# Performance work log

Measured on AMD Instinct MI355X. Metric: run time of the kernel, lower is better.

The kernel has to match this reference:

```python
import jax, jax.numpy as jnp
import numpy as np

B, S, D, H, DK, DV = 2, 2048, 1024, 16, 64, 64
NEG_INF = -2.0**32 + 1.0  # matches torch module's self.inf


def setup_inputs() -> dict:
    key = jax.random.key(0)
    ks = jax.random.split(key, 9)
    sc = 0.02
    x = jax.random.normal(ks[0], (B, S, D), jnp.float32)
    Wq = jax.random.normal(ks[1], (D, H * DK), jnp.float32) * sc
    bq = jax.random.normal(ks[2], (H * DK,), jnp.float32) * sc
    Wk = jax.random.normal(ks[3], (D, H * DK), jnp.float32) * sc
    bk = jax.random.normal(ks[4], (H * DK,), jnp.float32) * sc
    Wv = jax.random.normal(ks[5], (D, H * DV), jnp.float32) * sc
    bv = jax.random.normal(ks[6], (H * DV,), jnp.float32) * sc
    Wo = jax.random.normal(ks[7], (H * DV, D), jnp.float32) * sc
    bo = jax.random.normal(ks[8], (D,), jnp.float32) * sc
    return {"x": x, "Wq": Wq, "bq": bq, "Wk": Wk, "bk": bk,
            "Wv": Wv, "bv": bv, "Wo": Wo, "bo": bo}


def reference(x, Wq, bq, Wk, bk, Wv, bv, Wo, bo):
    # stage == 'train' path: causal mask applied.
    b, s, _ = x.shape
    # chunk(heads, dim=-1) + cat(dim=0) in torch == per-head split; equivalent
    # math expressed as [B, S, H, d] with head-batched einsums.
    q = (x @ Wq + bq).reshape(b, s, H, DK)
    k = (x @ Wk + bk).reshape(b, s, H, DK)
    v = (x @ Wv + bv).reshape(b, s, H, DV)
    # NOTE: original module does NOT scale by 1/sqrt(dk) — stay faithful.
    score = jnp.einsum('bqhd,bkhd->bhqk', q, k)  # [B, H, S, S]
    causal = jnp.tril(jnp.ones((s, s), dtype=bool))
    score = jnp.where(causal, score, NEG_INF)
    attn = jax.nn.softmax(score, axis=-1)
    ctx = jnp.einsum('bhqk,bkhd->bqhd', attn, v).reshape(b, s, H * DV)
    return ctx @ Wo + bo
```

## Files before the change

kernel.cpp:

```cpp
#include <hip/hip_runtime.h>
#include <stdint.h>

typedef unsigned short u16;
typedef __bf16 bf16_t;
typedef bf16_t bf16x8 __attribute__((ext_vector_type(8)));
typedef float f32x4 __attribute__((ext_vector_type(4)));

#define SB 2048
#define DMODEL 1024
#define NH 16
#define HD 64

__device__ __forceinline__ u16 f2bf(float f) {
  union { float f; uint32_t u; } v; v.f = f;
  uint32_t u = v.u;
  return (u16)((u + 0x7FFFu + ((u >> 16) & 1u)) >> 16);
}

__device__ __forceinline__ void gload16(const void* g, void* l) {
  __builtin_amdgcn_global_load_lds((const __attribute__((address_space(1))) void*)g,
                                   (__attribute__((address_space(3))) void*)l, 16, 0, 0);
}


__global__ __launch_bounds__(256) void k_cvt_x(const float* __restrict__ x, u16* __restrict__ xb) {
  int i = blockIdx.x * 256 + threadIdx.x;
  float4 v = ((const float4*)x)[i];
  uint2 o;
  o.x = (unsigned)f2bf(v.x) | ((unsigned)f2bf(v.y) << 16);
  o.y = (unsigned)f2bf(v.z) | ((unsigned)f2bf(v.w) << 16);
  ((uint2*)xb)[i] = o;
}

__global__ __launch_bounds__(256) void k_transpose_w(
    const float* __restrict__ W0, const float* __restrict__ W1,
    const float* __restrict__ W2, const float* __restrict__ W3,
    u16* __restrict__ T0, u16* __restrict__ T1,
    u16* __restrict__ T2, u16* __restrict__ T3) {
  __shared__ float tile[32][33];
  int mat = blockIdx.z;
  const float* W = (mat == 0) ? W0 : (mat == 1) ? W1 : (mat == 2) ? W2 : W3;
  u16* T = (mat == 0) ? T0 : (mat == 1) ? T1 : (mat == 2) ? T2 : T3;
  int r0 = blockIdx.y * 32, c0 = blockIdx.x * 32;
  int tx = threadIdx.x & 31, ty = threadIdx.x >> 5;
#pragma unroll
  for (int j = 0; j < 4; ++j)
    tile[ty + j * 8][tx] = W[(size_t)(r0 + ty + j * 8) * DMODEL + c0 + tx];
  __syncthreads();
#pragma unroll
  for (int j = 0; j < 4; ++j)
    T[(size_t)(c0 + ty + j * 8) * DMODEL + r0 + tx] = f2bf(tile[tx][ty + j * 8]);
}


__device__ __forceinline__ void gemm_loop(const u16* __restrict__ A, const u16* __restrict__ Bt,
                                          u16* As, u16* Bs, f32x4 (&acc)[4][4], int m0) {
  const int t = threadIdx.x, w = t >> 6, lane = t & 63;
  const int l15 = lane & 15, grp = lane >> 4;
  const int wr = w >> 1, wc = w & 1;
#pragma unroll
  for (int i = 0; i < 4; ++i)
#pragma unroll
    for (int j = 0; j < 4; ++j) acc[i][j] = (f32x4){0.f, 0.f, 0.f, 0.f};

  for (int ks = 0; ks < 16; ++ks) {
    const int k0 = ks * 64;
#pragma unroll
    for (int j = 0; j < 4; ++j) {
      int glin = (w * 4 + j) * 64 + lane;
      int row = glin >> 3;
      int g = (glin & 7) ^ (row & 7);
      gload16(A + (size_t)(m0 + row) * DMODEL + k0 + g * 8, (char*)As + (size_t)(w * 4 + j) * 1024);
      gload16(Bt + (size_t)row * DMODEL + k0 + g * 8, (char*)Bs + (size_t)(w * 4 + j) * 1024);
    }
    __syncthreads();
#pragma unroll
    for (int kk = 0; kk < 2; ++kk) {
      bf16x8 af[4], bfr[4];
#pragma unroll
      for (int i = 0; i < 4; ++i) {
        int row = wr * 64 + i * 16 + l15;
        int g = (4 * kk + grp) ^ (row & 7);
        af[i] = *(const bf16x8*)((const char*)As + row * 128 + (g << 4));
      }
#pragma unroll
      for (int j = 0; j < 4; ++j) {
        int row = wc * 64 + j * 16 + l15;
        int g = (4 * kk + grp) ^ (row & 7);
        bfr[j] = *(const bf16x8*)((const char*)Bs + row * 128 + (g << 4));
      }
#pragma unroll
      for (int i = 0; i < 4; ++i)
#pragma unroll
        for (int j = 0; j < 4; ++j)
          acc[i][j] = __builtin_amdgcn_mfma_f32_16x16x32_bf16(af[i], bfr[j], acc[i][j], 0, 0, 0);
    }
    __syncthreads();
  }
}

__global__ __launch_bounds__(256) void k_gemm_qk(
    const u16* __restrict__ xb,
    const u16* __restrict__ WqT, const u16* __restrict__ WkT,
    const float* __restrict__ bq, const float* __restrict__ bk,
    u16* __restrict__ Qg, u16* __restrict__ Kg) {
  __shared__ u16 As[128 * 64];
  __shared__ u16 Bs[128 * 64];
  const int nt = blockIdx.x, mt = blockIdx.y;
  const int mat = nt >> 3, n0 = (nt & 7) * 128;
  const u16* Bt = mat ? WkT : WqT;
  const float* bias = mat ? bk : bq;
  u16* out = mat ? Kg : Qg;

  f32x4 acc[4][4];
  gemm_loop(xb, Bt + (size_t)n0 * DMODEL, As, Bs, acc, mt * 128);

  const int t = threadIdx.x, w = t >> 6, lane = t & 63;
  const int l15 = lane & 15, grp = lane >> 4;
  const int wr = w >> 1, wc = w & 1;
#pragma unroll
  for (int i = 0; i < 4; ++i)
#pragma unroll
    for (int j = 0; j < 4; ++j)
#pragma unroll
      for (int r = 0; r < 4; ++r) {
        int mrow = mt * 128 + wr * 64 + i * 16 + 4 * grp + r;
        int ncol = n0 + wc * 64 + j * 16 + l15;
        float v = acc[i][j][r] + bias[ncol];
        int b = mrow >> 11, s2 = mrow & 2047, h = ncol >> 6, d2 = ncol & 63;
        out[((((size_t)b * NH + h) * SB + s2) << 6) + d2] = f2bf(v);
      }
}

__global__ __launch_bounds__(256) void k_gemm_vt(
    const u16* __restrict__ xb, const u16* __restrict__ WvT,
    const float* __restrict__ bv, u16* __restrict__ VTg) {
  __shared__ u16 As[128 * 64];
  __shared__ u16 Bs[128 * 64];
  const int nt = blockIdx.x, mt = blockIdx.y;
  const int n0 = nt * 128;

  f32x4 acc[4][4];
  gemm_loop(WvT, xb + (size_t)n0 * DMODEL, As, Bs, acc, mt * 128);

  const int t = threadIdx.x, w = t >> 6, lane = t & 63;
  const int l15 = lane & 15, grp = lane >> 4;
  const int wr = w >> 1, wc = w & 1;
#pragma unroll
  for (int i = 0; i < 4; ++i)
#pragma unroll
    for (int j = 0; j < 4; ++j)
#pragma unroll
      for (int r = 0; r < 4; ++r) {
        int mrow = mt * 128 + wr * 64 + i * 16 + 4 * grp + r;
        int ncol = n0 + wc * 64 + j * 16 + l15;
        float v = acc[i][j][r] + bv[mrow];
        int b2 = ncol >> 11, key = ncol & 2047, h2 = mrow >> 6, vc = mrow & 63;
        VTg[((((size_t)b2 * NH + h2) << 6) + vc) * 2048 + key] = f2bf(v);
      }
}

__global__ __launch_bounds__(256) void k_gemm_o(
    const u16* __restrict__ ctx, const u16* __restrict__ WoT,
    const float* __restrict__ bo, float* __restrict__ out) {
  __shared__ u16 As[128 * 64];
  __shared__ u16 Bs[128 * 64];
  const int nt = blockIdx.x, mt = blockIdx.y;
  const int n0 = nt * 128;

  f32x4 acc[4][4];
  gemm_loop(ctx, WoT + (size_t)n0 * DMODEL, As, Bs, acc, mt * 128);

  const int t = threadIdx.x, w = t >> 6, lane = t & 63;
  const int l15 = lane & 15, grp = lane >> 4;
  const int wr = w >> 1, wc = w & 1;
#pragma unroll
  for (int i = 0; i < 4; ++i)
#pragma unroll
    for (int j = 0; j < 4; ++j)
#pragma unroll
      for (int r = 0; r < 4; ++r) {
        int mrow = mt * 128 + wr * 64 + i * 16 + 4 * grp + r;
        int ncol = n0 + wc * 64 + j * 16 + l15;
        out[(size_t)mrow * DMODEL + ncol] = acc[i][j][r] + bo[ncol];
      }
}


__global__ __launch_bounds__(256) void k_flash(const u16* __restrict__ Qg,
                                               const u16* __restrict__ Kg,
                                               const u16* __restrict__ VTg,
                                               u16* __restrict__ ctx) {
  __shared__ u16 Ks[2][64 * 64];
  __shared__ u16 VTs[2][64 * 64];
  __shared__ u16 Ps[4][16 * 64];
  const int pi = blockIdx.x, bh = blockIdx.y;
  const int t = threadIdx.x, w = t >> 6, lane = t & 63;
  const int l15 = lane & 15, grp = lane >> 4;
  const size_t bhS = (size_t)bh * SB;
  const u16* Kb = Kg + (bhS << 6);
  const u16* Vb = VTg + (bhS << 6);
  const int b = bh >> 4, h = bh & 15;

#pragma unroll 1
  for (int ph = 0; ph < 2; ++ph) {
    const int qt = ph ? 31 - pi : pi;
    const int qb = qt * 64;
    bf16x8 qf[2];
#pragma unroll
    for (int c = 0; c < 2; ++c)
      qf[c] = *(const bf16x8*)(Qg + ((bhS + qb + w * 16 + l15) << 6) + 32 * c + 8 * grp);
    f32x4 acc[4];
    float plsum[4];
#pragma unroll
    for (int ct = 0; ct < 4; ++ct) acc[ct] = (f32x4){0.f, 0.f, 0.f, 0.f};
#pragma unroll
    for (int j = 0; j < 4; ++j) plsum[j] = 0.f;

#pragma unroll
    for (int j = 0; j < 2; ++j) {
      int glin = w * 128 + j * 64 + lane;
      int row = glin >> 3;
      int g = (glin & 7) ^ (row & 7);
      gload16(Kb + ((size_t)row << 6) + g * 8, (char*)Ks[0] + w * 2048 + j * 1024);
      gload16(Vb + ((size_t)row << 11) + g * 8, (char*)VTs[0] + w * 2048 + j * 1024);
    }
    __syncthreads();
    int cur = 0;
    for (int kt = 0; kt <= qt; ++kt) {
      if (kt < qt) {
        const int kb2 = (kt + 1) * 64;
#pragma unroll
        for (int j = 0; j < 2; ++j) {
          int glin = w * 128 + j * 64 + lane;
          int row = glin >> 3;
          int g = (glin & 7) ^ (row & 7);
          gload16(Kb + ((size_t)(kb2 + row) << 6) + g * 8,
                  (char*)Ks[cur ^ 1] + w * 2048 + j * 1024);
          gload16(Vb + ((size_t)row << 11) + kb2 + g * 8,
                  (char*)VTs[cur ^ 1] + w * 2048 + j * 1024);
        }
      }
      f32x4 sc[4];
#pragma unroll
      for (int ct = 0; ct < 4; ++ct) {
        sc[ct] = (f32x4){0.f, 0.f, 0.f, 0.f};
#pragma unroll
        for (int c = 0; c < 2; ++c) {
          int row = ct * 16 + l15;
          int g = (4 * c + grp) ^ (row & 7);
          bf16x8 kf = *(const bf16x8*)((const char*)Ks[cur] + row * 128 + (g << 4));
          sc[ct] = __builtin_amdgcn_mfma_f32_16x16x32_bf16(qf[c], kf, sc[ct], 0, 0, 0);
        }
      }
      if (kt == qt) {
#pragma unroll
        for (int ct = 0; ct < 4; ++ct)
#pragma unroll
          for (int j = 0; j < 4; ++j) {
            int key = ct * 16 + l15, r = w * 16 + 4 * grp + j;
            if (key > r) sc[ct][j] = -1e30f;
          }
      }
#pragma unroll
      for (int ct = 0; ct < 4; ++ct)
#pragma unroll
        for (int j = 0; j < 4; ++j) {
          float p = __expf(sc[ct][j] - 32.0f);
          plsum[j] += p;
          int r = 4 * grp + j, cc = ct * 16 + l15;
          *(u16*)((char*)Ps[w] + r * 128 + (((cc >> 3) ^ (r & 7)) << 4) + (cc & 7) * 2) = f2bf(p);
        }
      asm volatile("s_waitcnt lgkmcnt(0)" ::: "memory");
      __builtin_amdgcn_sched_barrier(0);
#pragma unroll
      for (int ct = 0; ct < 4; ++ct) {
#pragma unroll
        for (int c2 = 0; c2 < 2; ++c2) {
          int pg = (4 * c2 + grp) ^ (l15 & 7);
          bf16x8 pf = *(const bf16x8*)((const char*)Ps[w] + l15 * 128 + (pg << 4));
          int vrow = ct * 16 + l15;
          int vg = (4 * c2 + grp) ^ (vrow & 7);
          bf16x8 vf = *(const bf16x8*)((const char*)VTs[cur] + vrow * 128 + (vg << 4));
          acc[ct] = __builtin_amdgcn_mfma_f32_16x16x32_bf16(pf, vf, acc[ct], 0, 0, 0);
        }
      }
      __syncthreads();
      cur ^= 1;
    }
#pragma unroll
    for (int j = 0; j < 4; ++j) {
#pragma unroll
      for (int d = 1; d < 16; d <<= 1) plsum[j] += __shfl_xor(plsum[j], d, 64);
      float inv = 1.f / plsum[j];
      int rg = qb + w * 16 + 4 * grp + j;
#pragma unroll
      for (int ct = 0; ct < 4; ++ct) {
        int col = h * 64 + ct * 16 + l15;
        ctx[((size_t)b * SB + rg) * DMODEL + col] = f2bf(acc[ct][j] * inv);
      }
    }
  }
}


extern "C" void kernel_launch(void* const* d_in, const int* in_sizes, int n_in,
                              void* d_out, int out_size, void* d_ws, size_t ws_size,
                              hipStream_t stream) {
  const float* x  = (const float*)d_in[0];
  const float* Wq = (const float*)d_in[1];
  const float* bq = (const float*)d_in[2];
  const float* Wk = (const float*)d_in[3];
  const float* bk = (const float*)d_in[4];
  const float* Wv = (const float*)d_in[5];
  const float* bv = (const float*)d_in[6];
  const float* Wo = (const float*)d_in[7];
  const float* bo = (const float*)d_in[8];
  float* out = (float*)d_out;

  char* ws = (char*)d_ws;
  u16* xb  = (u16*)(ws);
  u16* WqT = (u16*)(ws + (8ull  << 20));
  u16* WkT = (u16*)(ws + (10ull << 20));
  u16* WvT = (u16*)(ws + (12ull << 20));
  u16* WoT = (u16*)(ws + (14ull << 20));
  u16* Qg  = (u16*)(ws + (16ull << 20));
  u16* Kg  = (u16*)(ws + (24ull << 20));
  u16* VTg = (u16*)(ws + (32ull << 20));
  u16* ctx = (u16*)(ws + (40ull << 20));

  hipLaunchKernelGGL(k_cvt_x, dim3(4096), dim3(256), 0, stream, x, xb);
  hipLaunchKernelGGL(k_transpose_w, dim3(32, 32, 4), dim3(256), 0, stream,
                     Wq, Wk, Wv, Wo, WqT, WkT, WvT, WoT);
  hipLaunchKernelGGL(k_gemm_qk, dim3(16, 32), dim3(256), 0, stream,
                     xb, WqT, WkT, bq, bk, Qg, Kg);
  hipLaunchKernelGGL(k_gemm_vt, dim3(32, 8), dim3(256), 0, stream, xb, WvT, bv, VTg);
  hipLaunchKernelGGL(k_flash, dim3(16, 32), dim3(256), 0, stream, Qg, Kg, VTg, ctx);
  hipLaunchKernelGGL(k_gemm_o, dim3(8, 32), dim3(256), 0, stream, ctx, WoT, bo, out);
}
```

Baseline: 128.3 us.

## Double-buffer GEMM loads, merge QKV GEMMs, and widen flash blocks

The GEMM main loop now double-buffers its LDS tiles, so the next K-slice's global-to-LDS loads are issued before the MFMAs on the current slice. This replaces the old load-sync-compute pattern. The Q/K and V^T projection GEMMs are merged into one 768-block launch with a swizzled block id meant to group blocks per XCD. The flash attention kernel now uses 512 threads covering a 128-row query tile, with per-wave causal masking and an XCD-aware mapping from block to (batch, head). Together these aim to hide load latency, cut launch overhead and improve L2 locality, at the cost of doubled LDS per block and a larger flash block that may lower occupancy.

```diff
diff --git a/kernel.cpp b/kernel.cpp
--- a/kernel.cpp
+++ b/kernel.cpp
@@ -53,8 +53,8 @@
 }
 
 
-__device__ __forceinline__ void gemm_loop(const u16* __restrict__ A, const u16* __restrict__ Bt,
-                                          u16* As, u16* Bs, f32x4 (&acc)[4][4], int m0) {
+__device__ __forceinline__ void gemm_db(const u16* __restrict__ A, const u16* __restrict__ Bt,
+                                        u16* As, u16* Bs, f32x4 (&acc)[4][4]) {
   const int t = threadIdx.x, w = t >> 6, lane = t & 63;
   const int l15 = lane & 15, grp = lane >> 4;
   const int wr = w >> 1, wc = w & 1;
@@ -63,17 +63,25 @@
 #pragma unroll
     for (int j = 0; j < 4; ++j) acc[i][j] = (f32x4){0.f, 0.f, 0.f, 0.f};
 
+#define STAGE_G(BUF, K0)                                                                     \
+  do {                                                                                       \
+    _Pragma("unroll") for (int j_ = 0; j_ < 4; ++j_) {                                       \
+      int glin_ = (w * 4 + j_) * 64 + lane;                                                  \
+      int row_ = glin_ >> 3;                                                                 \
+      int g_ = (glin_ & 7) ^ (row_ & 7);                                                     \
+      gload16(A + (size_t)row_ * DMODEL + (K0) + g_ * 8,                                     \
+              (char*)As + (BUF) * 16384 + glin_ * 16);                                       \
+      gload16(Bt + (size_t)row_ * DMODEL + (K0) + g_ * 8,                                    \
+              (char*)Bs + (BUF) * 16384 + glin_ * 16);                                       \
+    }                                                                                        \
+  } while (0)
+
+  STAGE_G(0, 0);
+  __syncthreads();
+  int cur = 0;
+#pragma unroll 1
   for (int ks = 0; ks < 16; ++ks) {
-    const int k0 = ks * 64;
-#pragma unroll
-    for (int j = 0; j < 4; ++j) {
-      int glin = (w * 4 + j) * 64 + lane;
-      int row = glin >> 3;
-      int g = (glin & 7) ^ (row & 7);
-      gload16(A + (size_t)(m0 + row) * DMODEL + k0 + g * 8, (char*)As + (size_t)(w * 4 + j) * 1024);
-      gload16(Bt + (size_t)row * DMODEL + k0 + g * 8, (char*)Bs + (size_t)(w * 4 + j) * 1024);
-    }
-    __syncthreads();
+    if (ks < 15) STAGE_G(cur ^ 1, (ks + 1) * 64);
 #pragma unroll
     for (int kk = 0; kk < 2; ++kk) {
       bf16x8 af[4], bfr[4];
@@ -81,13 +89,13 @@
       for (int i = 0; i < 4; ++i) {
         int row = wr * 64 + i * 16 + l15;
         int g = (4 * kk + grp) ^ (row & 7);
-        af[i] = *(const bf16x8*)((const char*)As + row * 128 + (g << 4));
+        af[i] = *(const bf16x8*)((const char*)As + cur * 16384 + row * 128 + (g << 4));
       }
 #pragma unroll
       for (int j = 0; j < 4; ++j) {
         int row = wc * 64 + j * 16 + l15;
         int g = (4 * kk + grp) ^ (row & 7);
-        bfr[j] = *(const bf16x8*)((const char*)Bs + row * 128 + (g << 4));
+        bfr[j] = *(const bf16x8*)((const char*)Bs + cur * 16384 + row * 128 + (g << 4));
       }
 #pragma unroll
       for (int i = 0; i < 4; ++i)
@@ -96,24 +104,40 @@
           acc[i][j] = __builtin_amdgcn_mfma_f32_16x16x32_bf16(af[i], bfr[j], acc[i][j], 0, 0, 0);
     }
     __syncthreads();
+    cur ^= 1;
   }
-}
-
-__global__ __launch_bounds__(256) void k_gemm_qk(
-    const u16* __restrict__ xb,
-    const u16* __restrict__ WqT, const u16* __restrict__ WkT,
-    const float* __restrict__ bq, const float* __restrict__ bk,
-    u16* __restrict__ Qg, u16* __restrict__ Kg) {
-  __shared__ u16 As[128 * 64];
-  __shared__ u16 Bs[128 * 64];
-  const int nt = blockIdx.x, mt = blockIdx.y;
-  const int mat = nt >> 3, n0 = (nt & 7) * 128;
-  const u16* Bt = mat ? WkT : WqT;
-  const float* bias = mat ? bk : bq;
-  u16* out = mat ? Kg : Qg;
+#undef STAGE_G
+}
+
+
+__global__ __launch_bounds__(256) void k_qkv(
+    const u16* __restrict__ xb, const u16* __restrict__ WqT, const u16* __restrict__ WkT,
+    const u16* __restrict__ WvT, const float* __restrict__ bq, const float* __restrict__ bk,
+    const float* __restrict__ bv, u16* __restrict__ Qg, u16* __restrict__ Kg,
+    u16* __restrict__ VTg) {
+  __shared__ u16 As[2][8192];
+  __shared__ u16 Bs[2][8192];
+  int id = blockIdx.x;
+  id = (id & 7) * 96 + (id >> 3);
+  const int role = id >> 8;
+  int mt, nt;
+  const u16 *Abase, *Bbase;
+  if (role < 2) {
+    int r = id & 255;
+    mt = r >> 3;
+    nt = r & 7;
+    Abase = xb + (size_t)mt * 128 * DMODEL;
+    Bbase = (role ? WkT : WqT) + (size_t)nt * 128 * DMODEL;
+  } else {
+    int r = id & 255;
+    mt = r >> 5;
+    nt = r & 31;
+    Abase = WvT + (size_t)mt * 128 * DMODEL;
+    Bbase = xb + (size_t)nt * 128 * DMODEL;
+  }
 
   f32x4 acc[4][4];
-  gemm_loop(xb, Bt + (size_t)n0 * DMODEL, As, Bs, acc, mt * 128);
+  gemm_db(Abase, Bbase, As[0], Bs[0], acc);
 
   const int t = threadIdx.x, w = t >> 6, lane = t & 63;
   const int l15 = lane & 15, grp = lane >> 4;
@@ -124,24 +148,32 @@
     for (int j = 0; j < 4; ++j)
 #pragma unroll
       for (int r = 0; r < 4; ++r) {
-        int mrow = mt * 128 + wr * 64 + i * 16 + 4 * grp + r;
-        int ncol = n0 + wc * 64 + j * 16 + l15;
-        float v = acc[i][j][r] + bias[ncol];
-        int b = mrow >> 11, s2 = mrow & 2047, h = ncol >> 6, d2 = ncol & 63;
-        out[((((size_t)b * NH + h) * SB + s2) << 6) + d2] = f2bf(v);
-      }
-}
-
-__global__ __launch_bounds__(256) void k_gemm_vt(
-    const u16* __restrict__ xb, const u16* __restrict__ WvT,
-    const float* __restrict__ bv, u16* __restrict__ VTg) {
-  __shared__ u16 As[128 * 64];
-  __shared__ u16 Bs[128 * 64];
+        int mr = mt * 128 + wr * 64 + i * 16 + 4 * grp + r;
+        int nc = nt * 128 + wc * 64 + j * 16 + l15;
+        float v = acc[i][j][r];
+        if (role < 2) {
+          float vb = v + (role ? bk[nc] : bq[nc]);
+          int b_ = mr >> 11, s_ = mr & 2047, h_ = nc >> 6, d_ = nc & 63;
+          u16* out = role ? Kg : Qg;
+          out[((((size_t)b_ * NH + h_) * SB + s_) << 6) + d_] = f2bf(vb);
+        } else {
+          float vb = v + bv[mr];
+          int b2 = nc >> 11, key = nc & 2047, h2 = mr >> 6, vc = mr & 63;
+          VTg[((((size_t)b2 * NH + h2) << 6) + vc) * SB + key] = f2bf(vb);
+        }
+      }
+}
+
+
+__global__ __launch_bounds__(256) void k_gemm_o(
+    const u16* __restrict__ ctx, const u16* __restrict__ WoT,
+    const float* __restrict__ bo, float* __restrict__ out) {
+  __shared__ u16 As[2][8192];
+  __shared__ u16 Bs[2][8192];
   const int nt = blockIdx.x, mt = blockIdx.y;
-  const int n0 = nt * 128;
 
   f32x4 acc[4][4];
-  gemm_loop(WvT, xb + (size_t)n0 * DMODEL, As, Bs, acc, mt * 128);
+  gemm_db(ctx + (size_t)mt * 128 * DMODEL, WoT + (size_t)nt * 128 * DMODEL, As[0], Bs[0], acc);
 
   const int t = threadIdx.x, w = t >> 6, lane = t & 63;
   const int l15 = lane & 15, grp = lane >> 4;
@@ -153,48 +185,23 @@
 #pragma unroll
       for (int r = 0; r < 4; ++r) {
         int mrow = mt * 128 + wr * 64 + i * 16 + 4 * grp + r;
-        int ncol = n0 + wc * 64 + j * 16 + l15;
-        float v = acc[i][j][r] + bv[mrow];
-        int b2 = ncol >> 11, key = ncol & 2047, h2 = mrow >> 6, vc = mrow & 63;
-        VTg[((((size_t)b2 * NH + h2) << 6) + vc) * 2048 + key] = f2bf(v);
-      }
-}
-
-__global__ __launch_bounds__(256) void k_gemm_o(
-    const u16* __restrict__ ctx, const u16* __restrict__ WoT,
-    const float* __restrict__ bo, float* __restrict__ out) {
-  __shared__ u16 As[128 * 64];
-  __shared__ u16 Bs[128 * 64];
-  const int nt = blockIdx.x, mt = blockIdx.y;
-  const int n0 = nt * 128;
-
-  f32x4 acc[4][4];
-  gemm_loop(ctx, WoT + (size_t)n0 * DMODEL, As, Bs, acc, mt * 128);
-
-  const int t = threadIdx.x, w = t >> 6, lane = t & 63;
-  const int l15 = lane & 15, grp = lane >> 4;
-  const int wr = w >> 1, wc = w & 1;
-#pragma unroll
-  for (int i = 0; i < 4; ++i)
-#pragma unroll
-    for (int j = 0; j < 4; ++j)
-#pragma unroll
-      for (int r = 0; r < 4; ++r) {
-        int mrow = mt * 128 + wr * 64 + i * 16 + 4 * grp + r;
-        int ncol = n0 + wc * 64 + j * 16 + l15;
+        int ncol = nt * 128 + wc * 64 + j * 16 + l15;
         out[(size_t)mrow * DMODEL + ncol] = acc[i][j][r] + bo[ncol];
       }
 }
 
 
-__global__ __launch_bounds__(256) void k_flash(const u16* __restrict__ Qg,
+__global__ __launch_bounds__(512) void k_flash(const u16* __restrict__ Qg,
                                                const u16* __restrict__ Kg,
                                                const u16* __restrict__ VTg,
                                                u16* __restrict__ ctx) {
-  __shared__ u16 Ks[2][64 * 64];
-  __shared__ u16 VTs[2][64 * 64];
-  __shared__ u16 Ps[4][16 * 64];
-  const int pi = blockIdx.x, bh = blockIdx.y;
+  __shared__ u16 Ks[2][4096];
+  __shared__ u16 VTs[2][4096];
+  __shared__ u16 Ps[8][1024];
+  const int linb = blockIdx.x;
+  const int xcd = linb & 7, idx = linb >> 3;
+  const int bh = xcd + ((idx & 3) << 3);
+  const int pi = idx >> 2;
   const int t = threadIdx.x, w = t >> 6, lane = t & 63;
   const int l15 = lane & 15, grp = lane >> 4;
   const size_t bhS = (size_t)bh * SB;
@@ -204,8 +211,9 @@
 
 #pragma unroll 1
   for (int ph = 0; ph < 2; ++ph) {
-    const int qt = ph ? 31 - pi : pi;
-    const int qb = qt * 64;
+    const int qt = ph ? 15 - pi : pi;
+    const int qb = qt * 128;
+    const int nkt = 2 * qt + 2;
     bf16x8 qf[2];
 #pragma unroll
     for (int c = 0; c < 2; ++c)
@@ -217,29 +225,20 @@
 #pragma unroll
     for (int j = 0; j < 4; ++j) plsum[j] = 0.f;
 
-#pragma unroll
-    for (int j = 0; j < 2; ++j) {
-      int glin = w * 128 + j * 64 + lane;
-      int row = glin >> 3;
-      int g = (glin & 7) ^ (row & 7);
-      gload16(Kb + ((size_t)row << 6) + g * 8, (char*)Ks[0] + w * 2048 + j * 1024);
-      gload16(Vb + ((size_t)row << 11) + g * 8, (char*)VTs[0] + w * 2048 + j * 1024);
+    {
+      int row = t >> 3, g = (t & 7) ^ (row & 7);
+      gload16(Kb + ((size_t)row << 6) + g * 8, (char*)Ks[0] + t * 16);
+      gload16(Vb + ((size_t)row << 11) + g * 8, (char*)VTs[0] + t * 16);
     }
     __syncthreads();
     int cur = 0;
-    for (int kt = 0; kt <= qt; ++kt) {
-      if (kt < qt) {
-        const int kb2 = (kt + 1) * 64;
-#pragma unroll
-        for (int j = 0; j < 2; ++j) {
-          int glin = w * 128 + j * 64 + lane;
-          int row = glin >> 3;
-          int g = (glin & 7) ^ (row & 7);
-          gload16(Kb + ((size_t)(kb2 + row) << 6) + g * 8,
-                  (char*)Ks[cur ^ 1] + w * 2048 + j * 1024);
-          gload16(Vb + ((size_t)row << 11) + kb2 + g * 8,
-                  (char*)VTs[cur ^ 1] + w * 2048 + j * 1024);
-        }
+    for (int kt = 0; kt < nkt; ++kt) {
+      const int kb = kt * 64;
+      if (kt + 1 < nkt) {
+        int row = t >> 3, g = (t & 7) ^ (row & 7);
+        int kb2 = kb + 64;
+        gload16(Kb + ((size_t)(kb2 + row) << 6) + g * 8, (char*)Ks[cur ^ 1] + t * 16);
+        gload16(Vb + ((size_t)row << 11) + kb2 + g * 8, (char*)VTs[cur ^ 1] + t * 16);
       }
       f32x4 sc[4];
 #pragma unroll
@@ -253,12 +252,12 @@
           sc[ct] = __builtin_amdgcn_mfma_f32_16x16x32_bf16(qf[c], kf, sc[ct], 0, 0, 0);
         }
       }
-      if (kt == qt) {
+      if (kb + 63 >= qb + w * 16) {
 #pragma unroll
         for (int ct = 0; ct < 4; ++ct)
 #pragma unroll
           for (int j = 0; j < 4; ++j) {
-            int key = ct * 16 + l15, r = w * 16 + 4 * grp + j;
+            int key = kb + ct * 16 + l15, r = qb + w * 16 + 4 * grp + j;
             if (key > r) sc[ct][j] = -1e30f;
           }
       }
@@ -332,9 +331,8 @@
   hipLaunchKernelGGL(k_cvt_x, dim3(4096), dim3(256), 0, stream, x, xb);
   hipLaunchKernelGGL(k_transpose_w, dim3(32, 32, 4), dim3(256), 0, stream,
                      Wq, Wk, Wv, Wo, WqT, WkT, WvT, WoT);
-  hipLaunchKernelGGL(k_gemm_qk, dim3(16, 32), dim3(256), 0, stream,
-                     xb, WqT, WkT, bq, bk, Qg, Kg);
-  hipLaunchKernelGGL(k_gemm_vt, dim3(32, 8), dim3(256), 0, stream, xb, WvT, bv, VTg);
-  hipLaunchKernelGGL(k_flash, dim3(16, 32), dim3(256), 0, stream, Qg, Kg, VTg, ctx);
+  hipLaunchKernelGGL(k_qkv, dim3(768), dim3(256), 0, stream,
+                     xb, WqT, WkT, WvT, bq, bk, bv, Qg, Kg, VTg);
+  hipLaunchKernelGGL(k_flash, dim3(256), dim3(512), 0, stream, Qg, Kg, VTg, ctx);
   hipLaunchKernelGGL(k_gemm_o, dim3(8, 32), dim3(256), 0, stream, ctx, WoT, bo, out);
 }
```

Result: slower. 132.2 us (+3.0%).
